# Optimization experiments

Hardware: AMD Instinct MI355X
Metric: run time of the kernel (lower is better)

The kernel has to match this reference:

```python
import jax, jax.numpy as jnp
import numpy as np

B, C, F = 4, 3, 5
HO, WO = 256, 256
HI, WI = HO + F - 1, WO + F - 1


def setup_inputs() -> dict:
    key = jax.random.key(0)
    k = jax.random.split(key, 6)
    return {
        "tensorInput": jax.random.normal(k[0], (B, C, HI, WI), dtype=jnp.float32),
        "tensorVertical": jax.random.uniform(k[1], (B, F, HO, WO), dtype=jnp.float32),
        "tensorHorizontal": jax.random.uniform(k[2], (B, F, HO, WO), dtype=jnp.float32),
        "tensorOffsetX": jax.random.normal(k[3], (B, F * F, HO, WO), dtype=jnp.float32),
        "tensorOffsetY": jax.random.normal(k[4], (B, F * F, HO, WO), dtype=jnp.float32),
        "tensorMask": jax.random.uniform(k[5], (B, F * F, HO, WO), dtype=jnp.float32),
    }


def _dsepconv(inp, vertical, horizontal, offset_x, offset_y, mask):
    b, c, hin, win = inp.shape
    f = vertical.shape[1]
    ho, wo = vertical.shape[2], vertical.shape[3]
    half = (f - 1) / 2.0

    fy = jnp.arange(f, dtype=inp.dtype).reshape(f, 1, 1, 1)
    fx = jnp.arange(f, dtype=inp.dtype).reshape(1, f, 1, 1)
    hg = jnp.arange(ho, dtype=inp.dtype).reshape(1, 1, ho, 1)
    wg = jnp.arange(wo, dtype=inp.dtype).reshape(1, 1, 1, wo)

    off_y = offset_y.reshape(b, f, f, ho, wo)  # note: code uses offset_y for delta_x
    off_x = offset_x.reshape(b, f, f, ho, wo)  # and offset_x for delta_y

    # sample positions per tap, [B,F,F,Ho,Wo]
    px = jnp.clip(off_y + wg + fx - half + 1.0, 0.0, win - 1)
    py = jnp.clip(off_x + hg + fy - half + 1.0, 0.0, hin - 1)

    left_f = jnp.floor(px)
    top_f = jnp.floor(py)
    wx = 1.0 - (px - left_f)  # bilinear weights
    wy = 1.0 - (py - top_f)

    l = left_f.astype(jnp.int32)
    t = top_f.astype(jnp.int32)
    r = jnp.minimum(l + 1, win - 1)
    btm = jnp.minimum(t + 1, hin - 1)

    def gather(img, yi, xi):
        return img[:, yi, xi]

    g = jax.vmap(gather)
    v_tl = g(inp, t, l)
    v_tr = g(inp, t, r)
    v_bl = g(inp, btm, l)
    v_br = g(inp, btm, r)

    wx_ = wx[:, None]  # add channel axis -> [B,1,F,F,Ho,Wo]
    wy_ = wy[:, None]
    val = (v_tl * wx_ * wy_ + v_tr * (1 - wx_) * wy_
           + v_bl * wx_ * (1 - wy_) + v_br * (1 - wx_) * (1 - wy_))

    # separable filter x mask per tap: [B,F,F,Ho,Wo]
    w_tap = vertical[:, :, None] * horizontal[:, None, :] * mask.reshape(b, f, f, ho, wo)
    # accumulate over the F*F taps
    return jnp.sum(val * w_tap[:, None], axis=(2, 3))  # [B,C,Ho,Wo]


def reference(tensorInput, tensorVertical, tensorHorizontal, tensorOffsetX, tensorOffsetY, tensorMask):
    return _dsepconv(tensorInput, tensorVertical, tensorHorizontal,
                     tensorOffsetX, tensorOffsetY, tensorMask)
```

## Files before the change

### kernel.cpp

```cpp
#include <hip/hip_runtime.h>
#include <hip/hip_fp16.h>

constexpr int B  = 4;
constexpr int C  = 3;
constexpr int F  = 5;
constexpr int HO = 256;
constexpr int WO = 256;
constexpr int HI = HO + F - 1;
constexpr int WI = WO + F - 1;
constexpr int P  = HO * WO;
constexpr int FF = F * F;
constexpr int PI = HI * WI;

constexpr int TROWS = 17;
constexpr int TCOLS = 143;
constexpr int TSTRIDE = 149;
constexpr int TN = TROWS * TCOLS;
constexpr int AMAX = (TROWS - 2) * TSTRIDE + (TCOLS - 2);

__device__ __forceinline__ float2 ld2(const float* p) {
    return *reinterpret_cast<const float2*>(p);
}

__device__ __forceinline__ uint2 pack3(float a, float b, float c) {
    __half2 ab = __floats2half2_rn(a, b);
    __half2 cz = __floats2half2_rn(c, 0.0f);
    uint2 r;
    r.x = *reinterpret_cast<const unsigned int*>(&ab);
    r.y = *reinterpret_cast<const unsigned int*>(&cz);
    return r;
}

__device__ __forceinline__ void fmacc(uint2 v, float w,
                                      float& a0, float& a1, float& a2) {
    __half2 ab = *reinterpret_cast<const __half2*>(&v.x);
    __half2 cz = *reinterpret_cast<const __half2*>(&v.y);
    a0 += __half2float(__low2half(ab))  * w;
    a1 += __half2float(__high2half(ab)) * w;
    a2 += __half2float(__low2half(cz))  * w;
}

__global__ __launch_bounds__(256, 4) void dsepconv_kernel(
    const float* __restrict__ inp,
    const float* __restrict__ vert,
    const float* __restrict__ horz,
    const float* __restrict__ offX,
    const float* __restrict__ offY,
    const float* __restrict__ mask,
    float* __restrict__ out)
{
    __shared__ uint2 tileq[TROWS * TSTRIDE];
    __shared__ float red[2][3][128];

    const int tid  = threadIdx.x;
    const int lane = tid & 63;
    const int wave = tid >> 6;
    const int wrow = wave >> 1;
    const int half = wave & 1;

    const int bx   = blockIdx.x;
    const int x0   = (bx & 1) * 128;
    const int y0   = ((bx >> 1) & 127) * 2;
    const int b    = bx >> 8;

    const float* in0 = inp + (size_t)b * C * PI;
    const float* in1 = in0 + PI;
    const float* in2 = in1 + PI;

    const int x   = x0 + 2 * lane;
    const int y   = y0 + wrow;
    const int pix = y * WO + x;

    const float* offXb = offX + (size_t)b * FF * P + pix;
    const float* offYb = offY + (size_t)b * FF * P + pix;
    const float* maskb = mask + (size_t)b * FF * P + pix;
    const float* vb    = vert + (size_t)b * F * P + pix;
    const float* hb    = horz + (size_t)b * F * P + pix;

    const int k0 = half ? 12 : 0;
    const int k1 = half ? 25 : 12;

    float2 oy, ox, m, h, v;
    {
        const int i = k0 / F, j = k0 - (k0 / F) * F;
        oy = ld2(offYb + (size_t)k0 * P);
        ox = ld2(offXb + (size_t)k0 * P);
        m  = ld2(maskb + (size_t)k0 * P);
        h  = ld2(hb + (size_t)j * P);
        v  = ld2(vb + (size_t)i * P);
    }

    const int ry0 = y0 - 6;
    const int cx0 = x0 - 6;
#pragma unroll 4
    for (int e = tid; e < TN; e += 256) {
        int trow = e / TCOLS;
        int tcol = e - trow * TCOLS;
        int gy = min(max(ry0 + trow, 0), HI - 1);
        int gx = min(max(cx0 + tcol, 0), WI - 1);
        int g = gy * WI + gx;
        tileq[trow * TSTRIDE + tcol] = pack3(in0[g], in1[g], in2[g]);
    }
    __syncthreads();

    float acc0a = 0.f, acc1a = 0.f, acc2a = 0.f;
    float acc0b = 0.f, acc1b = 0.f, acc2b = 0.f;

#pragma unroll 1
    for (int k = k0; k < k1; ++k) {
        const int i = k / F;
        const int j = k - i * F;

        const int kn  = (k + 1 < k1) ? k + 1 : k;
        const int in_ = kn / F;
        const int jn  = kn - in_ * F;
        float2 oy_n = ld2(offYb + (size_t)kn * P);
        float2 ox_n = ld2(offXb + (size_t)kn * P);
        float2 m_n  = ld2(maskb + (size_t)kn * P);
        float2 h_n  = ld2(hb + (size_t)jn * P);
        float2 v_n  = ld2(vb + (size_t)in_ * P);

        float pya = fminf(fmaxf(ox.x + (float)(y + i - 1), 0.0f), (float)(HI - 1));
        float pyb = fminf(fmaxf(ox.y + (float)(y + i - 1), 0.0f), (float)(HI - 1));
        float pxa = fminf(fmaxf(oy.x + (float)(x + j - 1), 0.0f), (float)(WI - 1));
        float pxb = fminf(fmaxf(oy.y + (float)(x + j), 0.0f), (float)(WI - 1));

        float lfa = floorf(pxa), tfa = floorf(pya);
        float lfb = floorf(pxb), tfb = floorf(pyb);
        int la = (int)lfa, ta = (int)tfa;
        int lb = (int)lfb, tb = (int)tfb;
        float wxa = 1.0f - (pxa - lfa), wya = 1.0f - (pya - tfa);
        float wxb = 1.0f - (pxb - lfb), wyb = 1.0f - (pyb - tfb);

        int lta = ta - ry0, lla = la - cx0;
        int ltb = tb - ry0, llb = lb - cx0;
        bool oka = ((unsigned)lta <= TROWS - 2) & ((unsigned)lla <= TCOLS - 2);
        bool okb = ((unsigned)ltb <= TROWS - 2) & ((unsigned)llb <= TCOLS - 2);

        int aa = min(max(lta * TSTRIDE + lla, 0), AMAX);
        int ab = min(max(ltb * TSTRIDE + llb, 0), AMAX);

        uint2 ga0 = tileq[aa];
        uint2 ga1 = tileq[aa + 1];
        uint2 ga2 = tileq[aa + TSTRIDE];
        uint2 ga3 = tileq[aa + TSTRIDE + 1];
        uint2 gb0 = tileq[ab];
        uint2 gb1 = tileq[ab + 1];
        uint2 gb2 = tileq[ab + TSTRIDE];
        uint2 gb3 = tileq[ab + TSTRIDE + 1];

        if (__any(!(oka & okb))) {
            if (!oka) {
                int r  = min(la + 1, WI - 1);
                int bt = min(ta + 1, HI - 1);
                int o0 = ta * WI + la, o1 = ta * WI + r;
                int o2 = bt * WI + la, o3 = bt * WI + r;
                ga0 = pack3(in0[o0], in1[o0], in2[o0]);
                ga1 = pack3(in0[o1], in1[o1], in2[o1]);
                ga2 = pack3(in0[o2], in1[o2], in2[o2]);
                ga3 = pack3(in0[o3], in1[o3], in2[o3]);
            }
            if (!okb) {
                int r  = min(lb + 1, WI - 1);
                int bt = min(tb + 1, HI - 1);
                int o0 = tb * WI + lb, o1 = tb * WI + r;
                int o2 = bt * WI + lb, o3 = bt * WI + r;
                gb0 = pack3(in0[o0], in1[o0], in2[o0]);
                gb1 = pack3(in0[o1], in1[o1], in2[o1]);
                gb2 = pack3(in0[o2], in1[o2], in2[o2]);
                gb3 = pack3(in0[o3], in1[o3], in2[o3]);
            }
        }

        float wA   = v.x * h.x * m.x;
        float wywA = wya * wA;
        float wbwA = wA - wywA;
        float wtlA = wxa * wywA;
        float wtrA = wywA - wtlA;
        float wblA = wxa * wbwA;
        float wbrA = wbwA - wblA;

        float wB   = v.y * h.y * m.y;
        float wywB = wyb * wB;
        float wbwB = wB - wywB;
        float wtlB = wxb * wywB;
        float wtrB = wywB - wtlB;
        float wblB = wxb * wbwB;
        float wbrB = wbwB - wblB;

        fmacc(ga0, wtlA, acc0a, acc1a, acc2a);
        fmacc(ga1, wtrA, acc0a, acc1a, acc2a);
        fmacc(ga2, wblA, acc0a, acc1a, acc2a);
        fmacc(ga3, wbrA, acc0a, acc1a, acc2a);
        fmacc(gb0, wtlB, acc0b, acc1b, acc2b);
        fmacc(gb1, wtrB, acc0b, acc1b, acc2b);
        fmacc(gb2, wblB, acc0b, acc1b, acc2b);
        fmacc(gb3, wbrB, acc0b, acc1b, acc2b);

        oy = oy_n; ox = ox_n; m = m_n; h = h_n; v = v_n;
    }

    if (half) {
        *reinterpret_cast<float2*>(&red[wrow][0][2 * lane]) = make_float2(acc0a, acc0b);
        *reinterpret_cast<float2*>(&red[wrow][1][2 * lane]) = make_float2(acc1a, acc1b);
        *reinterpret_cast<float2*>(&red[wrow][2][2 * lane]) = make_float2(acc2a, acc2b);
    }
    __syncthreads();

    if (!half) {
        float* ob = out + (size_t)b * C * P + pix;
        float2 r0 = *reinterpret_cast<const float2*>(&red[wrow][0][2 * lane]);
        float2 r1 = *reinterpret_cast<const float2*>(&red[wrow][1][2 * lane]);
        float2 r2 = *reinterpret_cast<const float2*>(&red[wrow][2][2 * lane]);
        *reinterpret_cast<float2*>(&ob[0])     = make_float2(acc0a + r0.x, acc0b + r0.y);
        *reinterpret_cast<float2*>(&ob[P])     = make_float2(acc1a + r1.x, acc1b + r1.y);
        *reinterpret_cast<float2*>(&ob[2 * P]) = make_float2(acc2a + r2.x, acc2b + r2.y);
    }
}

extern "C" void kernel_launch(void* const* d_in, const int* in_sizes, int n_in,
                              void* d_out, int out_size, void* d_ws, size_t ws_size,
                              hipStream_t stream) {
    const float* inp  = (const float*)d_in[0];
    const float* vert = (const float*)d_in[1];
    const float* horz = (const float*)d_in[2];
    const float* offX = (const float*)d_in[3];
    const float* offY = (const float*)d_in[4];
    const float* mask = (const float*)d_in[5];
    float* out = (float*)d_out;

    dim3 block(256);
    dim3 grid(B * (HO / 2) * (WO / 128));
    dsepconv_kernel<<<grid, block, 0, stream>>>(inp, vert, horz, offX, offY, mask, out);
}
```

Measured before the change: 23.53 us.

## Split taps across four waves with narrower 64-column tiles

Each block now covers a 2x64 pixel tile instead of 2x128, and the 25 taps are split four ways across the waves instead of two. This doubles the grid and shrinks the shared input tile, so more blocks fit per CU (launch bound raised to 6). The cost is a larger halo overhead for each output pixel in the staged tile and a three-way shared-memory reduction in place of a single add.

```diff
diff --git a/kernel.cpp b/kernel.cpp
--- a/kernel.cpp
+++ b/kernel.cpp
@@ -13,8 +13,8 @@
 constexpr int PI = HI * WI;
 
 constexpr int TROWS = 17;
-constexpr int TCOLS = 143;
-constexpr int TSTRIDE = 149;
+constexpr int TCOLS = 79;
+constexpr int TSTRIDE = 85;
 constexpr int TN = TROWS * TCOLS;
 constexpr int AMAX = (TROWS - 2) * TSTRIDE + (TCOLS - 2);
 
@@ -40,7 +40,7 @@
     a2 += __half2float(__low2half(cz))  * w;
 }
 
-__global__ __launch_bounds__(256, 4) void dsepconv_kernel(
+__global__ __launch_bounds__(256, 6) void dsepconv_kernel(
     const float* __restrict__ inp,
     const float* __restrict__ vert,
     const float* __restrict__ horz,
@@ -49,26 +49,26 @@
     const float* __restrict__ mask,
     float* __restrict__ out)
 {
-    __shared__ uint2 tileq[TROWS * TSTRIDE];
-    __shared__ float red[2][3][128];
+    __shared__ uint2 tileq[(TROWS - 1) * TSTRIDE + TCOLS];
+    __shared__ float red[3][3][128];
 
     const int tid  = threadIdx.x;
     const int lane = tid & 63;
     const int wave = tid >> 6;
-    const int wrow = wave >> 1;
-    const int half = wave & 1;
+    const int row  = lane >> 5;
+    const int xl   = lane & 31;
 
     const int bx   = blockIdx.x;
-    const int x0   = (bx & 1) * 128;
-    const int y0   = ((bx >> 1) & 127) * 2;
-    const int b    = bx >> 8;
+    const int x0   = (bx & 3) * 64;
+    const int y0   = ((bx >> 2) & 127) * 2;
+    const int b    = bx >> 9;
 
     const float* in0 = inp + (size_t)b * C * PI;
     const float* in1 = in0 + PI;
     const float* in2 = in1 + PI;
 
-    const int x   = x0 + 2 * lane;
-    const int y   = y0 + wrow;
+    const int x   = x0 + 2 * xl;
+    const int y   = y0 + row;
     const int pix = y * WO + x;
 
     const float* offXb = offX + (size_t)b * FF * P + pix;
@@ -77,8 +77,8 @@
     const float* vb    = vert + (size_t)b * F * P + pix;
     const float* hb    = horz + (size_t)b * F * P + pix;
 
-    const int k0 = half ? 12 : 0;
-    const int k1 = half ? 25 : 12;
+    const int k0 = wave * 6;
+    const int k1 = (wave == 3) ? FF : k0 + 6;
 
     float2 oy, ox, m, h, v;
     {
@@ -200,21 +200,34 @@
         oy = oy_n; ox = ox_n; m = m_n; h = h_n; v = v_n;
     }
 
-    if (half) {
-        *reinterpret_cast<float2*>(&red[wrow][0][2 * lane]) = make_float2(acc0a, acc0b);
-        *reinterpret_cast<float2*>(&red[wrow][1][2 * lane]) = make_float2(acc1a, acc1b);
-        *reinterpret_cast<float2*>(&red[wrow][2][2 * lane]) = make_float2(acc2a, acc2b);
+    const int p = row * 64 + 2 * xl;
+    if (wave != 0) {
+        *reinterpret_cast<float2*>(&red[wave - 1][0][p]) = make_float2(acc0a, acc0b);
+        *reinterpret_cast<float2*>(&red[wave - 1][1][p]) = make_float2(acc1a, acc1b);
+        *reinterpret_cast<float2*>(&red[wave - 1][2][p]) = make_float2(acc2a, acc2b);
     }
     __syncthreads();
 
-    if (!half) {
+    if (wave == 0) {
         float* ob = out + (size_t)b * C * P + pix;
-        float2 r0 = *reinterpret_cast<const float2*>(&red[wrow][0][2 * lane]);
-        float2 r1 = *reinterpret_cast<const float2*>(&red[wrow][1][2 * lane]);
-        float2 r2 = *reinterpret_cast<const float2*>(&red[wrow][2][2 * lane]);
-        *reinterpret_cast<float2*>(&ob[0])     = make_float2(acc0a + r0.x, acc0b + r0.y);
-        *reinterpret_cast<float2*>(&ob[P])     = make_float2(acc1a + r1.x, acc1b + r1.y);
-        *reinterpret_cast<float2*>(&ob[2 * P]) = make_float2(acc2a + r2.x, acc2b + r2.y);
+        float2 r00 = *reinterpret_cast<const float2*>(&red[0][0][p]);
+        float2 r01 = *reinterpret_cast<const float2*>(&red[1][0][p]);
+        float2 r02 = *reinterpret_cast<const float2*>(&red[2][0][p]);
+        float2 r10 = *reinterpret_cast<const float2*>(&red[0][1][p]);
+        float2 r11 = *reinterpret_cast<const float2*>(&red[1][1][p]);
+        float2 r12 = *reinterpret_cast<const float2*>(&red[2][1][p]);
+        float2 r20 = *reinterpret_cast<const float2*>(&red[0][2][p]);
+        float2 r21 = *reinterpret_cast<const float2*>(&red[1][2][p]);
+        float2 r22 = *reinterpret_cast<const float2*>(&red[2][2][p]);
+        *reinterpret_cast<float2*>(&ob[0]) =
+            make_float2(acc0a + r00.x + r01.x + r02.x,
+                        acc0b + r00.y + r01.y + r02.y);
+        *reinterpret_cast<float2*>(&ob[P]) =
+            make_float2(acc1a + r10.x + r11.x + r12.x,
+                        acc1b + r10.y + r11.y + r12.y);
+        *reinterpret_cast<float2*>(&ob[2 * P]) =
+            make_float2(acc2a + r20.x + r21.x + r22.x,
+                        acc2b + r20.y + r21.y + r22.y);
     }
 }
 
@@ -230,6 +243,6 @@
     float* out = (float*)d_out;
 
     dim3 block(256);
-    dim3 grid(B * (HO / 2) * (WO / 128));
+    dim3 grid(B * (HO / 2) * (WO / 64));
     dsepconv_kernel<<<grid, block, 0, stream>>>(inp, vert, horz, offX, offY, mask, out);
 }
```

Result: slower. 26.23 us (+11.5%).
